# Performance work log

Hardware: AMD Instinct MI355X
Metric: run time of the kernel (lower is better)

Reference implementation:

```python
import jax, jax.numpy as jnp
import numpy as np
import math

HEADS = 16
D_MODEL = 1024
HEAD_DIM = D_MODEL // HEADS
B, S = 2, 2048


def setup_inputs() -> dict:
    key = jax.random.key(0)
    ks = jax.random.split(key, 12)
    sc = 1.0 / math.sqrt(D_MODEL)
    inp = {
        "query": jax.random.normal(ks[0], (B, S, D_MODEL), jnp.float32),
        "key_t": jax.random.normal(ks[1], (B, S, D_MODEL), jnp.float32),
        "value": jax.random.normal(ks[2], (B, S, D_MODEL), jnp.float32),
        "mask": jax.random.randint(ks[3], (B, 1, 1, S), 0, 2, jnp.int32),
        "Wq": jax.random.normal(ks[4], (D_MODEL, D_MODEL), jnp.float32) * sc,
        "bq": jnp.zeros((D_MODEL,), jnp.float32),
        "Wk": jax.random.normal(ks[5], (D_MODEL, D_MODEL), jnp.float32) * sc,
        "bk": jnp.zeros((D_MODEL,), jnp.float32),
        "Wv": jax.random.normal(ks[6], (D_MODEL, D_MODEL), jnp.float32) * sc,
        "bv": jnp.zeros((D_MODEL,), jnp.float32),
        "Wo": jax.random.normal(ks[7], (D_MODEL, D_MODEL), jnp.float32) * sc,
        "bo": jnp.zeros((D_MODEL,), jnp.float32),
    }
    return inp


def _split_heads(x):
    # [B, S, D] -> [B, H, S, Dh]
    b, s, _ = x.shape
    return x.reshape(b, s, HEADS, HEAD_DIM).transpose(0, 2, 1, 3)


def reference(query, key_t, value, mask, Wq, bq, Wk, bk, Wv, bv, Wo, bo):
    # Linear projections (torch Linear: x @ W.T + b)
    q = _split_heads(query @ Wq.T + bq)
    k = _split_heads(key_t @ Wk.T + bk)
    v = _split_heads(value @ Wv.T + bv)
    # Scaled dot-product attention; scale by sqrt(head_dim) = query.size(-1) after split
    scores = jnp.einsum("bhqd,bhkd->bhqk", q, k) / math.sqrt(HEAD_DIM)
    scores = jnp.where(mask == 0, jnp.float32(-1e9), scores)
    prob = jax.nn.softmax(scores, axis=-1)
    # dropout is identity at inference
    attn = jnp.einsum("bhqk,bhkd->bhqd", prob, v)
    # [B, H, S, Dh] -> [B, S, D]
    attn = attn.transpose(0, 2, 1, 3).reshape(query.shape[0], -1, D_MODEL)
    return attn @ Wo.T + bo
```

## Files before the change

### kernel.cpp

```cpp
#include <hip/hip_runtime.h>
#include <hip/hip_bf16.h>

typedef __bf16 bf16;
typedef __bf16 bf16x8 __attribute__((ext_vector_type(8)));
typedef __bf16 bf16x4 __attribute__((ext_vector_type(4)));
typedef float  f32x4  __attribute__((ext_vector_type(4)));
typedef float  f32x16 __attribute__((ext_vector_type(16)));

#define AS1 __attribute__((address_space(1)))
#define AS3 __attribute__((address_space(3)))

__device__ __forceinline__ void gload_lds16(const bf16* g, bf16* l) {
    __builtin_amdgcn_global_load_lds((const AS1 unsigned int*)g,
                                     (AS3 unsigned int*)l, 16, 0, 0);
}

__global__ __launch_bounds__(256) void cast8_k(
    const float* __restrict__ s0, const float* __restrict__ s1,
    const float* __restrict__ s2, const float* __restrict__ s3,
    const float* __restrict__ s4, const float* __restrict__ s5,
    const float* __restrict__ s6,
    bf16* __restrict__ d0, bf16* __restrict__ d1, bf16* __restrict__ d2,
    bf16* __restrict__ d3, bf16* __restrict__ d4, bf16* __restrict__ d5,
    bf16* __restrict__ d6,
    const int* __restrict__ m, float* __restrict__ mb,
    int n_big, int n_small) {
    int z = blockIdx.z;
    int i = (blockIdx.x * 256 + threadIdx.x) * 8;
    if (z == 7) {
        if (i >= 4096) return;
        int4 a = *(const int4*)(m + i);
        int4 b = *(const int4*)(m + i + 4);
        float4 o0, o1;
        o0.x = (a.x == 0) ? -1.442695e9f : -17.3123405f;
        o0.y = (a.y == 0) ? -1.442695e9f : -17.3123405f;
        o0.z = (a.z == 0) ? -1.442695e9f : -17.3123405f;
        o0.w = (a.w == 0) ? -1.442695e9f : -17.3123405f;
        o1.x = (b.x == 0) ? -1.442695e9f : -17.3123405f;
        o1.y = (b.y == 0) ? -1.442695e9f : -17.3123405f;
        o1.z = (b.z == 0) ? -1.442695e9f : -17.3123405f;
        o1.w = (b.w == 0) ? -1.442695e9f : -17.3123405f;
        *(float4*)(mb + i) = o0;
        *(float4*)(mb + i + 4) = o1;
        return;
    }
    const float* s = (z == 0) ? s0 : (z == 1) ? s1 : (z == 2) ? s2
                   : (z == 3) ? s3 : (z == 4) ? s4 : (z == 5) ? s5 : s6;
    bf16* d = (z == 0) ? d0 : (z == 1) ? d1 : (z == 2) ? d2
            : (z == 3) ? d3 : (z == 4) ? d4 : (z == 5) ? d5 : d6;
    int n = (z < 3) ? n_big : n_small;
    if (i >= n) return;
    float4 a = *(const float4*)(s + i);
    float4 b = *(const float4*)(s + i + 4);
    bf16x8 o;
    o[0] = (bf16)a.x; o[1] = (bf16)a.y; o[2] = (bf16)a.z; o[3] = (bf16)a.w;
    o[4] = (bf16)b.x; o[5] = (bf16)b.y; o[6] = (bf16)b.z; o[7] = (bf16)b.w;
    *(bf16x8*)(d + i) = o;
}

template <typename OUT_T, bool TRANS>
__device__ __forceinline__ void gemm32_core(
    bf16* Asm, bf16* Bsm,
    const bf16* __restrict__ A, const bf16* __restrict__ W,
    const float* __restrict__ bias, OUT_T* __restrict__ C,
    int m0, int n0, int N, int K) {
    const int lane = threadIdx.x & 63;
    const int w = threadIdx.x >> 6;
    const int l31 = lane & 31;
    const int h = lane >> 5;
    const int x7 = l31 & 7;
    const int srow = lane >> 3;
    const int scol = ((lane & 7) ^ srow) * 8;
    const int wm = (w & 1) * 64;
    const int wn = (w >> 1) * 64;

    f32x16 acc[2][2] = {};

    for (int k0 = 0; k0 < K; k0 += 64) {
#pragma unroll
        for (int c = 0; c < 4; ++c) {
            int r = w * 32 + c * 8;
            gload_lds16(A + (size_t)(m0 + r + srow) * K + k0 + scol, &Asm[r * 64]);
            gload_lds16(W + (size_t)(n0 + r + srow) * K + k0 + scol, &Bsm[r * 64]);
        }
        __syncthreads();
#pragma unroll
        for (int step = 0; step < 4; ++step) {
            bf16x8 af[2], bfv[2];
#pragma unroll
            for (int i = 0; i < 2; ++i)
                af[i] = *(const bf16x8*)&Asm[(wm + i * 32 + l31) * 64 +
                                             (((step * 2 + h) ^ x7) * 8)];
#pragma unroll
            for (int j = 0; j < 2; ++j)
                bfv[j] = *(const bf16x8*)&Bsm[(wn + j * 32 + l31) * 64 +
                                              (((step * 2 + h) ^ x7) * 8)];
#pragma unroll
            for (int i = 0; i < 2; ++i)
#pragma unroll
                for (int j = 0; j < 2; ++j)
                    acc[i][j] = TRANS
                        ? __builtin_amdgcn_mfma_f32_32x32x16_bf16(bfv[j], af[i],
                                                                  acc[i][j], 0, 0, 0)
                        : __builtin_amdgcn_mfma_f32_32x32x16_bf16(af[i], bfv[j],
                                                                  acc[i][j], 0, 0, 0);
        }
        __syncthreads();
    }
    if (!TRANS) {
#pragma unroll
        for (int i = 0; i < 2; ++i)
#pragma unroll
            for (int j = 0; j < 2; ++j) {
                int col = n0 + wn + j * 32 + l31;
                float bv = bias[col];
#pragma unroll
                for (int g = 0; g < 4; ++g)
#pragma unroll
                    for (int rr = 0; rr < 4; ++rr) {
                        int row = m0 + wm + i * 32 + rr + g * 8 + 4 * h;
                        C[(size_t)row * N + col] =
                            (OUT_T)(acc[i][j][g * 4 + rr] + bv);
                    }
            }
    } else {
#pragma unroll
        for (int i = 0; i < 2; ++i) {
            int s = m0 + wm + i * 32 + l31;
            int b = s >> 11;
            int sl = s & 2047;
            int sp = (sl & ~12) | ((sl & 4) << 1) | ((sl & 8) >> 1);
#pragma unroll
            for (int j = 0; j < 2; ++j)
#pragma unroll
                for (int g = 0; g < 4; ++g) {
                    float4 bv4 = *(const float4*)&bias[n0 + wn + j * 32 + g * 8 + 4 * h];
#pragma unroll
                    for (int rr = 0; rr < 4; ++rr) {
                        int n = n0 + wn + j * 32 + g * 8 + 4 * h + rr;
                        C[(size_t)(b * 1024 + n) * 2048 + sp] =
                            (OUT_T)(acc[i][j][g * 4 + rr] + (&bv4.x)[rr]);
                    }
                }
        }
    }
}

__global__ __launch_bounds__(256) void gemm_qkv(
    const bf16* __restrict__ qb, const bf16* __restrict__ kb, const bf16* __restrict__ vb,
    const bf16* __restrict__ Wq, const bf16* __restrict__ Wk, const bf16* __restrict__ Wv,
    const float* __restrict__ bq, const float* __restrict__ bk, const float* __restrict__ bv,
    bf16* __restrict__ Qp, bf16* __restrict__ Kp, bf16* __restrict__ VpT) {
    __shared__ bf16 Asm[128 * 64];
    __shared__ bf16 Bsm[128 * 64];
    const int id = blockIdx.x;
    const int g = id % 24;
    const int m0 = (id / 24) * 128;
    const int z = g >> 3;
    const int n0 = (g & 7) * 128;
    if (z == 2) {
        gemm32_core<bf16, true>(Asm, Bsm, vb, Wv, bv, VpT, m0, n0, 1024, 1024);
    } else {
        const bf16* A = (z == 0) ? qb : kb;
        const bf16* W = (z == 0) ? Wq : Wk;
        const float* bi = (z == 0) ? bq : bk;
        bf16* C = (z == 0) ? Qp : Kp;
        gemm32_core<bf16, false>(Asm, Bsm, A, W, bi, C, m0, n0, 1024, 1024);
    }
}

__global__ __launch_bounds__(256) void gemm_out_fused(
    const bf16* __restrict__ Op, const float* __restrict__ Lp,
    const bf16* __restrict__ W, const float* __restrict__ bias,
    float* __restrict__ C) {
    __shared__ bf16 Asm[64 * 64];
    __shared__ bf16 Bsm[128 * 64];
    const int id = blockIdx.x;
    const int m0 = (id & 63) * 64;
    const int n0 = (id >> 6) * 128;
    const int lane = threadIdx.x & 63;
    const int w = threadIdx.x >> 6;
    const int l31 = lane & 31;
    const int h = lane >> 5;
    const int x7 = l31 & 7;
    const int srow = lane >> 3;
    const int l7 = lane & 7;
    const int scol = (l7 ^ srow) * 8;
    const int wm = (w & 1) * 32;
    const int wn = (w >> 1) * 64;

    f32x16 acc[2] = {};

    for (int k0 = 0; k0 < 1024; k0 += 64) {
#pragma unroll
        for (int c = 0; c < 2; ++c) {
            int r = w * 16 + c * 8;
            int row = m0 + r + srow;
            int colb = k0 + scol;
            int b = row >> 11, q = row & 2047;
            int hh = colb >> 6, d = colb & 63;
            size_t l0i = (size_t)(b * 16 + hh) * 2048 + q;
            bf16x8 v0 = *(const bf16x8*)&Op[l0i * 64 + d];
            bf16x8 v1 = *(const bf16x8*)&Op[(l0i + 32 * 2048) * 64 + d];
            float inv = 1.0f / (Lp[l0i] + Lp[l0i + 32 * 2048]);
            bf16x8 o;
#pragma unroll
            for (int i = 0; i < 8; ++i)
                o[i] = (bf16)(((float)v0[i] + (float)v1[i]) * inv);
            *(bf16x8*)&Asm[(r + srow) * 64 + l7 * 8] = o;
        }
#pragma unroll
        for (int c = 0; c < 4; ++c) {
            int r = w * 32 + c * 8;
            gload_lds16(W + (size_t)(n0 + r + srow) * 1024 + k0 + scol, &Bsm[r * 64]);
        }
        __syncthreads();
#pragma unroll
        for (int step = 0; step < 4; ++step) {
            bf16x8 af = *(const bf16x8*)&Asm[(wm + l31) * 64 +
                                             (((step * 2 + h) ^ x7) * 8)];
            bf16x8 bfv[2];
#pragma unroll
            for (int j = 0; j < 2; ++j)
                bfv[j] = *(const bf16x8*)&Bsm[(wn + j * 32 + l31) * 64 +
                                              (((step * 2 + h) ^ x7) * 8)];
#pragma unroll
            for (int j = 0; j < 2; ++j)
                acc[j] = __builtin_amdgcn_mfma_f32_32x32x16_bf16(af, bfv[j],
                                                                 acc[j], 0, 0, 0);
        }
        __syncthreads();
    }
#pragma unroll
    for (int j = 0; j < 2; ++j) {
        int col = n0 + wn + j * 32 + l31;
        float bv = bias[col];
#pragma unroll
        for (int g = 0; g < 4; ++g)
#pragma unroll
            for (int rr = 0; rr < 4; ++rr) {
                int row = m0 + wm + rr + g * 8 + 4 * h;
                C[(size_t)row * 1024 + col] = acc[j][g * 4 + rr] + bv;
            }
    }
}

__global__ __launch_bounds__(256, 2) void attn_k(
    const bf16* __restrict__ Qp, const bf16* __restrict__ Kp,
    const bf16* __restrict__ VpT, const float* __restrict__ mb,
    bf16* __restrict__ Opart, float* __restrict__ Lpart) {
    __shared__ bf16 KV[2][2][64 * 64];
    const int g = blockIdx.x;
    const int qb = g >> 6;
    const int bh = (g & 63) >> 1;
    const int sp = g & 1;
    const int b = bh >> 4, hh = bh & 15;
    const int lane = threadIdx.x & 63, w = threadIdx.x >> 6;
    const int l31 = lane & 31, h = lane >> 5;
    const int x7 = l31 & 7;
    const int srow = lane >> 3, scol = ((lane & 7) ^ srow) * 8;
    const float SC = 0.125f * 1.44269504f;
    const int q0 = qb * 256;
    const int k0 = sp * 1024;

    const bf16* Kg = Kp + (size_t)(b * 2048) * 1024 + hh * 64;
    const bf16* Vg = VpT + (size_t)bh * 64 * 2048;
    const float* mbb = mb + b * 2048;

    auto stage = [&](int buf, int kt) {
#pragma unroll
        for (int c = 0; c < 2; ++c) {
            int r = w * 16 + c * 8;
            gload_lds16(Kg + (size_t)(kt + r + srow) * 1024 + scol,
                        &KV[buf][0][r * 64]);
            gload_lds16(Vg + (size_t)(r + srow) * 2048 + kt + scol,
                        &KV[buf][1][r * 64]);
        }
    };
    stage(0, k0);

    bf16x8 qf[2][4];
#pragma unroll
    for (int qg = 0; qg < 2; ++qg) {
        const bf16* Qbase =
            Qp + (size_t)(b * 2048 + q0 + w * 64 + qg * 32 + l31) * 1024 + hh * 64;
#pragma unroll
        for (int step = 0; step < 4; ++step)
            qf[qg][step] = *(const bf16x8*)(Qbase + step * 16 + h * 8);
    }

    f32x16 o[2][2] = {};
    float lsum[2] = {0.0f, 0.0f};

    for (int it = 0; it < 16; ++it) {
        __syncthreads();
        if (it < 15) stage((it + 1) & 1, k0 + (it + 1) * 64);
        const bf16* Ks = KV[it & 1][0];
        const bf16* Vs = KV[it & 1][1];
        const int kt = k0 + it * 64;

        bf16x8 pa[2][4];
#pragma unroll
        for (int kg = 0; kg < 2; ++kg) {
            f32x16 z0 = {}, z1 = {};
#pragma unroll
            for (int step = 0; step < 4; ++step) {
                bf16x8 kf = *(const bf16x8*)&Ks[(kg * 32 + l31) * 64 +
                                                (((step * 2 + h) ^ x7) * 8)];
                z0 = __builtin_amdgcn_mfma_f32_32x32x16_bf16(kf, qf[0][step], z0, 0, 0, 0);
                z1 = __builtin_amdgcn_mfma_f32_32x32x16_bf16(kf, qf[1][step], z1, 0, 0, 0);
            }
#pragma unroll
            for (int g = 0; g < 4; ++g) {
                float4 bia = *(const float4*)&mbb[kt + kg * 32 + g * 8 + 4 * h];
#pragma unroll
                for (int qg = 0; qg < 2; ++qg) {
                    const f32x16& z = qg ? z1 : z0;
                    float p0 = __builtin_amdgcn_exp2f(fmaf(z[g * 4 + 0], SC, bia.x));
                    float p1 = __builtin_amdgcn_exp2f(fmaf(z[g * 4 + 1], SC, bia.y));
                    float p2 = __builtin_amdgcn_exp2f(fmaf(z[g * 4 + 2], SC, bia.z));
                    float p3 = __builtin_amdgcn_exp2f(fmaf(z[g * 4 + 3], SC, bia.w));
                    lsum[qg] += (p0 + p1) + (p2 + p3);
                    bf16x8& pf = pa[qg][kg * 2 + (g >> 1)];
                    int jb = (g & 1) * 4;
                    pf[jb + 0] = (bf16)p0;
                    pf[jb + 1] = (bf16)p1;
                    pf[jb + 2] = (bf16)p2;
                    pf[jb + 3] = (bf16)p3;
                }
            }
        }
#pragma unroll
        for (int t = 0; t < 2; ++t)
#pragma unroll
            for (int kk = 0; kk < 4; ++kk) {
                bf16x8 vf = *(const bf16x8*)&Vs[(t * 32 + l31) * 64 +
                                                (((kk * 2 + h) ^ x7) * 8)];
                o[0][t] = __builtin_amdgcn_mfma_f32_32x32x16_bf16(pa[0][kk], vf, o[0][t], 0, 0, 0);
                o[1][t] = __builtin_amdgcn_mfma_f32_32x32x16_bf16(pa[1][kk], vf, o[1][t], 0, 0, 0);
            }
    }

    const size_t pbase = (size_t)(sp * 32 + bh) * 2048;
#pragma unroll
    for (int qg = 0; qg < 2; ++qg) {
        float ls = lsum[qg] + __shfl_xor(lsum[qg], 32, 64);
        if (h == 0)
            Lpart[pbase + q0 + w * 64 + qg * 32 + l31] = ls;
#pragma unroll
        for (int t = 0; t < 2; ++t)
#pragma unroll
            for (int g = 0; g < 4; ++g)
#pragma unroll
                for (int rr = 0; rr < 4; ++rr) {
                    int q = q0 + w * 64 + qg * 32 + rr + g * 8 + 4 * h;
                    Opart[(pbase + q) * 64 + t * 32 + l31] =
                        (bf16)o[qg][t][g * 4 + rr];
                }
    }
}

extern "C" void kernel_launch(void* const* d_in, const int* in_sizes, int n_in,
                              void* d_out, int out_size, void* d_ws, size_t ws_size,
                              hipStream_t stream) {
    const float* q   = (const float*)d_in[0];
    const float* kt  = (const float*)d_in[1];
    const float* v   = (const float*)d_in[2];
    const int* mask  = (const int*)d_in[3];
    const float* Wq  = (const float*)d_in[4];
    const float* bq  = (const float*)d_in[5];
    const float* Wk  = (const float*)d_in[6];
    const float* bk  = (const float*)d_in[7];
    const float* Wv  = (const float*)d_in[8];
    const float* bv  = (const float*)d_in[9];
    const float* Wo  = (const float*)d_in[10];
    const float* bo  = (const float*)d_in[11];
    float* out = (float*)d_out;

    char* ws = (char*)d_ws;
    const size_t SZ_IN = 4096ull * 1024 * 2;
    const size_t SZ_W  = 1024ull * 1024 * 2;
    bf16* qb  = (bf16*)(ws + 0 * SZ_IN);
    bf16* kb  = (bf16*)(ws + 1 * SZ_IN);
    bf16* vb  = (bf16*)(ws + 2 * SZ_IN);
    bf16* Wqb = (bf16*)(ws + 3 * SZ_IN);
    bf16* Wkb = (bf16*)(ws + 3 * SZ_IN + 1 * SZ_W);
    bf16* Wvb = (bf16*)(ws + 3 * SZ_IN + 2 * SZ_W);
    bf16* Wob = (bf16*)(ws + 3 * SZ_IN + 3 * SZ_W);
    bf16* Qp  = (bf16*)(ws + 3 * SZ_IN + 4 * SZ_W);
    bf16* Kp  = (bf16*)(ws + 4 * SZ_IN + 4 * SZ_W);
    bf16* VpT = (bf16*)(ws + 5 * SZ_IN + 4 * SZ_W);
    float* mb = (float*)(ws + 6 * SZ_IN + 4 * SZ_W);
    char*  p0 = ws + 6 * SZ_IN + 4 * SZ_W + (1 << 20);
    bf16* Opart = (bf16*)p0;
    float* Lpart = (float*)(p0 + 2ull * 32 * 2048 * 64 * 2);

    const int NIN = 4096 * 1024, NW = 1024 * 1024;
    cast8_k<<<dim3(NIN / 2048, 1, 8), 256, 0, stream>>>(
        q, kt, v, Wq, Wk, Wv, Wo, qb, kb, vb, Wqb, Wkb, Wvb, Wob,
        mask, mb, NIN, NW);

    gemm_qkv<<<dim3(768), 256, 0, stream>>>(qb, kb, vb, Wqb, Wkb, Wvb,
                                            bq, bk, bv, Qp, Kp, VpT);
    attn_k<<<dim3(512), 256, 0, stream>>>(Qp, Kp, VpT, mb, Opart, Lpart);
    gemm_out_fused<<<dim3(512), 256, 0, stream>>>(Opart, Lpart, Wob, bo, out);
}
```

Before: 226.6 us.

## Split attention keys four ways and flatten the cast launch grid

The attention kernel now splits the key range into four 512-key partitions instead of two, which doubles the grid to 1024 blocks and raises the launch bound to 4 blocks per CU for more occupancy. The output GEMM now sums four partial outputs and normalizers when it loads its A tile. The cast kernel moves from a 3D grid with idle blocks to a flat grid sized exactly to the work. The cost is twice the partial-output traffic and more reduction loads in the output GEMM, and the tighter launch bound may cause register spills.

```diff
diff --git a/kernel.cpp b/kernel.cpp
--- a/kernel.cpp
+++ b/kernel.cpp
@@ -15,7 +15,7 @@
                                      (AS3 unsigned int*)l, 16, 0, 0);
 }
 
-__global__ __launch_bounds__(256) void cast8_k(
+__global__ __launch_bounds__(256) void cast_flat_k(
     const float* __restrict__ s0, const float* __restrict__ s1,
     const float* __restrict__ s2, const float* __restrict__ s3,
     const float* __restrict__ s4, const float* __restrict__ s5,
@@ -23,12 +23,10 @@
     bf16* __restrict__ d0, bf16* __restrict__ d1, bf16* __restrict__ d2,
     bf16* __restrict__ d3, bf16* __restrict__ d4, bf16* __restrict__ d5,
     bf16* __restrict__ d6,
-    const int* __restrict__ m, float* __restrict__ mb,
-    int n_big, int n_small) {
-    int z = blockIdx.z;
-    int i = (blockIdx.x * 256 + threadIdx.x) * 8;
-    if (z == 7) {
-        if (i >= 4096) return;
+    const int* __restrict__ m, float* __restrict__ mb) {
+    int bx = blockIdx.x;
+    if (bx >= 8192) {
+        int i = (bx - 8192) * 2048 + threadIdx.x * 8;
         int4 a = *(const int4*)(m + i);
         int4 b = *(const int4*)(m + i + 4);
         float4 o0, o1;
@@ -44,12 +42,13 @@
         *(float4*)(mb + i + 4) = o1;
         return;
     }
+    int z, i;
+    if (bx < 6144) { z = bx >> 11; i = (bx & 2047) * 2048 + threadIdx.x * 8; }
+    else { int r = bx - 6144; z = 3 + (r >> 9); i = (r & 511) * 2048 + threadIdx.x * 8; }
     const float* s = (z == 0) ? s0 : (z == 1) ? s1 : (z == 2) ? s2
                    : (z == 3) ? s3 : (z == 4) ? s4 : (z == 5) ? s5 : s6;
     bf16* d = (z == 0) ? d0 : (z == 1) ? d1 : (z == 2) ? d2
             : (z == 3) ? d3 : (z == 4) ? d4 : (z == 5) ? d5 : d6;
-    int n = (z < 3) ? n_big : n_small;
-    if (i >= n) return;
     float4 a = *(const float4*)(s + i);
     float4 b = *(const float4*)(s + i + 4);
     bf16x8 o;
@@ -200,13 +199,20 @@
             int b = row >> 11, q = row & 2047;
             int hh = colb >> 6, d = colb & 63;
             size_t l0i = (size_t)(b * 16 + hh) * 2048 + q;
-            bf16x8 v0 = *(const bf16x8*)&Op[l0i * 64 + d];
-            bf16x8 v1 = *(const bf16x8*)&Op[(l0i + 32 * 2048) * 64 + d];
-            float inv = 1.0f / (Lp[l0i] + Lp[l0i + 32 * 2048]);
+            float a8[8] = {};
+            float l = 0.0f;
+#pragma unroll
+            for (int sp = 0; sp < 4; ++sp) {
+                size_t idx = l0i + (size_t)sp * 32 * 2048;
+                bf16x8 v = *(const bf16x8*)&Op[idx * 64 + d];
+                l += Lp[idx];
+#pragma unroll
+                for (int i = 0; i < 8; ++i) a8[i] += (float)v[i];
+            }
+            float inv = 1.0f / l;
             bf16x8 o;
 #pragma unroll
-            for (int i = 0; i < 8; ++i)
-                o[i] = (bf16)(((float)v0[i] + (float)v1[i]) * inv);
+            for (int i = 0; i < 8; ++i) o[i] = (bf16)(a8[i] * inv);
             *(bf16x8*)&Asm[(r + srow) * 64 + l7 * 8] = o;
         }
 #pragma unroll
@@ -245,15 +251,15 @@
     }
 }
 
-__global__ __launch_bounds__(256, 2) void attn_k(
+__global__ __launch_bounds__(256, 4) void attn_k(
     const bf16* __restrict__ Qp, const bf16* __restrict__ Kp,
     const bf16* __restrict__ VpT, const float* __restrict__ mb,
     bf16* __restrict__ Opart, float* __restrict__ Lpart) {
     __shared__ bf16 KV[2][2][64 * 64];
     const int g = blockIdx.x;
-    const int qb = g >> 6;
-    const int bh = (g & 63) >> 1;
-    const int sp = g & 1;
+    const int qb = g >> 7;
+    const int bh = (g & 127) >> 2;
+    const int sp = g & 3;
     const int b = bh >> 4, hh = bh & 15;
     const int lane = threadIdx.x & 63, w = threadIdx.x >> 6;
     const int l31 = lane & 31, h = lane >> 5;
@@ -261,7 +267,7 @@
     const int srow = lane >> 3, scol = ((lane & 7) ^ srow) * 8;
     const float SC = 0.125f * 1.44269504f;
     const int q0 = qb * 256;
-    const int k0 = sp * 1024;
+    const int k0 = sp * 512;
 
     const bf16* Kg = Kp + (size_t)(b * 2048) * 1024 + hh * 64;
     const bf16* Vg = VpT + (size_t)bh * 64 * 2048;
@@ -292,9 +298,9 @@
     f32x16 o[2][2] = {};
     float lsum[2] = {0.0f, 0.0f};
 
-    for (int it = 0; it < 16; ++it) {
+    for (int it = 0; it < 8; ++it) {
         __syncthreads();
-        if (it < 15) stage((it + 1) & 1, k0 + (it + 1) * 64);
+        if (it < 7) stage((it + 1) & 1, k0 + (it + 1) * 64);
         const bf16* Ks = KV[it & 1][0];
         const bf16* Vs = KV[it & 1][1];
         const int kt = k0 + it * 64;
@@ -393,15 +399,13 @@
     float* mb = (float*)(ws + 6 * SZ_IN + 4 * SZ_W);
     char*  p0 = ws + 6 * SZ_IN + 4 * SZ_W + (1 << 20);
     bf16* Opart = (bf16*)p0;
-    float* Lpart = (float*)(p0 + 2ull * 32 * 2048 * 64 * 2);
-
-    const int NIN = 4096 * 1024, NW = 1024 * 1024;
-    cast8_k<<<dim3(NIN / 2048, 1, 8), 256, 0, stream>>>(
-        q, kt, v, Wq, Wk, Wv, Wo, qb, kb, vb, Wqb, Wkb, Wvb, Wob,
-        mask, mb, NIN, NW);
+    float* Lpart = (float*)(p0 + 4ull * 32 * 2048 * 64 * 2);
+
+    cast_flat_k<<<dim3(8194), 256, 0, stream>>>(
+        q, kt, v, Wq, Wk, Wv, Wo, qb, kb, vb, Wqb, Wkb, Wvb, Wob, mask, mb);
 
     gemm_qkv<<<dim3(768), 256, 0, stream>>>(qb, kb, vb, Wqb, Wkb, Wvb,
                                             bq, bk, bv, Qp, Kp, VpT);
-    attn_k<<<dim3(512), 256, 0, stream>>>(Qp, Kp, VpT, mb, Opart, Lpart);
+    attn_k<<<dim3(1024), 256, 0, stream>>>(Qp, Kp, VpT, mb, Opart, Lpart);
     gemm_out_fused<<<dim3(512), 256, 0, stream>>>(Opart, Lpart, Wob, bo, out);
 }
```

Measured after the change: 416.2 us. +83.7%, slower.

## Fuse activation fp32->bf16 cast into QKV GEMM and halve attention query tile

Applied to the files above, without the earlier changes.

Removes the separate cast of the three large fp32 activation tensors to bf16; the QKV GEMM now loads fp32 rows, converts them in registers and writes them into swizzled LDS, so only weights and the mask are pre-cast. This avoids writing and re-reading about 24 MB of bf16 intermediates, but A-tile loads become synchronous register round trips instead of direct global-to-LDS loads, and each A tile is re-read in fp32 by every N-tile block. Separately, the attention kernel processes 32 query rows per wave instead of 64 and launches twice as many blocks, with the occupancy hint removed. That lowers register pressure and adds parallelism at the cost of loading the K/V tiles twice as often.

```diff
diff --git a/kernel.cpp b/kernel.cpp
--- a/kernel.cpp
+++ b/kernel.cpp
@@ -15,20 +15,15 @@
                                      (AS3 unsigned int*)l, 16, 0, 0);
 }
 
-__global__ __launch_bounds__(256) void cast8_k(
-    const float* __restrict__ s0, const float* __restrict__ s1,
-    const float* __restrict__ s2, const float* __restrict__ s3,
-    const float* __restrict__ s4, const float* __restrict__ s5,
-    const float* __restrict__ s6,
-    bf16* __restrict__ d0, bf16* __restrict__ d1, bf16* __restrict__ d2,
-    bf16* __restrict__ d3, bf16* __restrict__ d4, bf16* __restrict__ d5,
-    bf16* __restrict__ d6,
-    const int* __restrict__ m, float* __restrict__ mb,
-    int n_big, int n_small) {
-    int z = blockIdx.z;
-    int i = (blockIdx.x * 256 + threadIdx.x) * 8;
-    if (z == 7) {
-        if (i >= 4096) return;
+__global__ __launch_bounds__(256) void cast_w_k(
+    const float* __restrict__ s3, const float* __restrict__ s4,
+    const float* __restrict__ s5, const float* __restrict__ s6,
+    bf16* __restrict__ d3, bf16* __restrict__ d4,
+    bf16* __restrict__ d5, bf16* __restrict__ d6,
+    const int* __restrict__ m, float* __restrict__ mb) {
+    int bx = blockIdx.x;
+    if (bx >= 2048) {
+        int i = (bx - 2048) * 2048 + threadIdx.x * 8;
         int4 a = *(const int4*)(m + i);
         int4 b = *(const int4*)(m + i + 4);
         float4 o0, o1;
@@ -44,12 +39,10 @@
         *(float4*)(mb + i + 4) = o1;
         return;
     }
-    const float* s = (z == 0) ? s0 : (z == 1) ? s1 : (z == 2) ? s2
-                   : (z == 3) ? s3 : (z == 4) ? s4 : (z == 5) ? s5 : s6;
-    bf16* d = (z == 0) ? d0 : (z == 1) ? d1 : (z == 2) ? d2
-            : (z == 3) ? d3 : (z == 4) ? d4 : (z == 5) ? d5 : d6;
-    int n = (z < 3) ? n_big : n_small;
-    if (i >= n) return;
+    int z = bx >> 9;
+    int i = (bx & 511) * 2048 + threadIdx.x * 8;
+    const float* s = (z == 0) ? s3 : (z == 1) ? s4 : (z == 2) ? s5 : s6;
+    bf16* d = (z == 0) ? d3 : (z == 1) ? d4 : (z == 2) ? d5 : d6;
     float4 a = *(const float4*)(s + i);
     float4 b = *(const float4*)(s + i + 4);
     bf16x8 o;
@@ -61,7 +54,7 @@
 template <typename OUT_T, bool TRANS>
 __device__ __forceinline__ void gemm32_core(
     bf16* Asm, bf16* Bsm,
-    const bf16* __restrict__ A, const bf16* __restrict__ W,
+    const float* __restrict__ A, const bf16* __restrict__ W,
     const float* __restrict__ bias, OUT_T* __restrict__ C,
     int m0, int n0, int N, int K) {
     const int lane = threadIdx.x & 63;
@@ -73,14 +66,28 @@
     const int scol = ((lane & 7) ^ srow) * 8;
     const int wm = (w & 1) * 64;
     const int wn = (w >> 1) * 64;
+    const int arow = threadIdx.x >> 3;
+    const int achk = threadIdx.x & 7;
 
     f32x16 acc[2][2] = {};
 
     for (int k0 = 0; k0 < K; k0 += 64) {
+#pragma unroll
+        for (int ps = 0; ps < 4; ++ps) {
+            int rr = ps * 32 + arow;
+            const float* src = A + (size_t)(m0 + rr) * K + k0 + achk * 8;
+            float4 a0 = *(const float4*)src;
+            float4 a1 = *(const float4*)(src + 4);
+            bf16x8 ob;
+            ob[0] = (bf16)a0.x; ob[1] = (bf16)a0.y;
+            ob[2] = (bf16)a0.z; ob[3] = (bf16)a0.w;
+            ob[4] = (bf16)a1.x; ob[5] = (bf16)a1.y;
+            ob[6] = (bf16)a1.z; ob[7] = (bf16)a1.w;
+            *(bf16x8*)&Asm[rr * 64 + ((achk ^ (rr & 7)) * 8)] = ob;
+        }
 #pragma unroll
         for (int c = 0; c < 4; ++c) {
             int r = w * 32 + c * 8;
-            gload_lds16(A + (size_t)(m0 + r + srow) * K + k0 + scol, &Asm[r * 64]);
             gload_lds16(W + (size_t)(n0 + r + srow) * K + k0 + scol, &Bsm[r * 64]);
         }
         __syncthreads();
@@ -147,7 +154,8 @@
 }
 
 __global__ __launch_bounds__(256) void gemm_qkv(
-    const bf16* __restrict__ qb, const bf16* __restrict__ kb, const bf16* __restrict__ vb,
+    const float* __restrict__ qf32, const float* __restrict__ kf32,
+    const float* __restrict__ vf32,
     const bf16* __restrict__ Wq, const bf16* __restrict__ Wk, const bf16* __restrict__ Wv,
     const float* __restrict__ bq, const float* __restrict__ bk, const float* __restrict__ bv,
     bf16* __restrict__ Qp, bf16* __restrict__ Kp, bf16* __restrict__ VpT) {
@@ -159,9 +167,9 @@
     const int z = g >> 3;
     const int n0 = (g & 7) * 128;
     if (z == 2) {
-        gemm32_core<bf16, true>(Asm, Bsm, vb, Wv, bv, VpT, m0, n0, 1024, 1024);
+        gemm32_core<bf16, true>(Asm, Bsm, vf32, Wv, bv, VpT, m0, n0, 1024, 1024);
     } else {
-        const bf16* A = (z == 0) ? qb : kb;
+        const float* A = (z == 0) ? qf32 : kf32;
         const bf16* W = (z == 0) ? Wq : Wk;
         const float* bi = (z == 0) ? bq : bk;
         bf16* C = (z == 0) ? Qp : Kp;
@@ -245,7 +253,7 @@
     }
 }
 
-__global__ __launch_bounds__(256, 2) void attn_k(
+__global__ __launch_bounds__(256) void attn_k(
     const bf16* __restrict__ Qp, const bf16* __restrict__ Kp,
     const bf16* __restrict__ VpT, const float* __restrict__ mb,
     bf16* __restrict__ Opart, float* __restrict__ Lpart) {
@@ -260,7 +268,7 @@
     const int x7 = l31 & 7;
     const int srow = lane >> 3, scol = ((lane & 7) ^ srow) * 8;
     const float SC = 0.125f * 1.44269504f;
-    const int q0 = qb * 256;
+    const int q0 = qb * 128;
     const int k0 = sp * 1024;
 
     const bf16* Kg = Kp + (size_t)(b * 2048) * 1024 + hh * 64;
@@ -279,18 +287,17 @@
     };
     stage(0, k0);
 
-    bf16x8 qf[2][4];
-#pragma unroll
-    for (int qg = 0; qg < 2; ++qg) {
+    bf16x8 qf[4];
+    {
         const bf16* Qbase =
-            Qp + (size_t)(b * 2048 + q0 + w * 64 + qg * 32 + l31) * 1024 + hh * 64;
+            Qp + (size_t)(b * 2048 + q0 + w * 32 + l31) * 1024 + hh * 64;
 #pragma unroll
         for (int step = 0; step < 4; ++step)
-            qf[qg][step] = *(const bf16x8*)(Qbase + step * 16 + h * 8);
-    }
-
-    f32x16 o[2][2] = {};
-    float lsum[2] = {0.0f, 0.0f};
+            qf[step] = *(const bf16x8*)(Qbase + step * 16 + h * 8);
+    }
+
+    f32x16 o[2] = {};
+    float lsum = 0.0f;
 
     for (int it = 0; it < 16; ++it) {
         __syncthreads();
@@ -299,35 +306,30 @@
         const bf16* Vs = KV[it & 1][1];
         const int kt = k0 + it * 64;
 
-        bf16x8 pa[2][4];
+        bf16x8 pa[4];
 #pragma unroll
         for (int kg = 0; kg < 2; ++kg) {
-            f32x16 z0 = {}, z1 = {};
+            f32x16 z = {};
 #pragma unroll
             for (int step = 0; step < 4; ++step) {
                 bf16x8 kf = *(const bf16x8*)&Ks[(kg * 32 + l31) * 64 +
                                                 (((step * 2 + h) ^ x7) * 8)];
-                z0 = __builtin_amdgcn_mfma_f32_32x32x16_bf16(kf, qf[0][step], z0, 0, 0, 0);
-                z1 = __builtin_amdgcn_mfma_f32_32x32x16_bf16(kf, qf[1][step], z1, 0, 0, 0);
-            }
-#pragma unroll
-            for (int g = 0; g < 4; ++g) {
-                float4 bia = *(const float4*)&mbb[kt + kg * 32 + g * 8 + 4 * h];
-#pragma unroll
-                for (int qg = 0; qg < 2; ++qg) {
-                    const f32x16& z = qg ? z1 : z0;
-                    float p0 = __builtin_amdgcn_exp2f(fmaf(z[g * 4 + 0], SC, bia.x));
-                    float p1 = __builtin_amdgcn_exp2f(fmaf(z[g * 4 + 1], SC, bia.y));
-                    float p2 = __builtin_amdgcn_exp2f(fmaf(z[g * 4 + 2], SC, bia.z));
-                    float p3 = __builtin_amdgcn_exp2f(fmaf(z[g * 4 + 3], SC, bia.w));
-                    lsum[qg] += (p0 + p1) + (p2 + p3);
-                    bf16x8& pf = pa[qg][kg * 2 + (g >> 1)];
-                    int jb = (g & 1) * 4;
-                    pf[jb + 0] = (bf16)p0;
-                    pf[jb + 1] = (bf16)p1;
-                    pf[jb + 2] = (bf16)p2;
-                    pf[jb + 3] = (bf16)p3;
-                }
+                z = __builtin_amdgcn_mfma_f32_32x32x16_bf16(kf, qf[step], z, 0, 0, 0);
+            }
+#pragma unroll
+            for (int gg = 0; gg < 4; ++gg) {
+                float4 bia = *(const float4*)&mbb[kt + kg * 32 + gg * 8 + 4 * h];
+                float p0 = __builtin_amdgcn_exp2f(fmaf(z[gg * 4 + 0], SC, bia.x));
+                float p1 = __builtin_amdgcn_exp2f(fmaf(z[gg * 4 + 1], SC, bia.y));
+                float p2 = __builtin_amdgcn_exp2f(fmaf(z[gg * 4 + 2], SC, bia.z));
+                float p3 = __builtin_amdgcn_exp2f(fmaf(z[gg * 4 + 3], SC, bia.w));
+                lsum += (p0 + p1) + (p2 + p3);
+                bf16x8& pf = pa[kg * 2 + (gg >> 1)];
+                int jb = (gg & 1) * 4;
+                pf[jb + 0] = (bf16)p0;
+                pf[jb + 1] = (bf16)p1;
+                pf[jb + 2] = (bf16)p2;
+                pf[jb + 3] = (bf16)p3;
             }
         }
 #pragma unroll
@@ -336,28 +338,24 @@
             for (int kk = 0; kk < 4; ++kk) {
                 bf16x8 vf = *(const bf16x8*)&Vs[(t * 32 + l31) * 64 +
                                                 (((kk * 2 + h) ^ x7) * 8)];
-                o[0][t] = __builtin_amdgcn_mfma_f32_32x32x16_bf16(pa[0][kk], vf, o[0][t], 0, 0, 0);
-                o[1][t] = __builtin_amdgcn_mfma_f32_32x32x16_bf16(pa[1][kk], vf, o[1][t], 0, 0, 0);
+                o[t] = __builtin_amdgcn_mfma_f32_32x32x16_bf16(pa[kk], vf, o[t], 0, 0, 0);
             }
     }
 
     const size_t pbase = (size_t)(sp * 32 + bh) * 2048;
-#pragma unroll
-    for (int qg = 0; qg < 2; ++qg) {
-        float ls = lsum[qg] + __shfl_xor(lsum[qg], 32, 64);
-        if (h == 0)
-            Lpart[pbase + q0 + w * 64 + qg * 32 + l31] = ls;
-#pragma unroll
-        for (int t = 0; t < 2; ++t)
-#pragma unroll
-            for (int g = 0; g < 4; ++g)
-#pragma unroll
-                for (int rr = 0; rr < 4; ++rr) {
-                    int q = q0 + w * 64 + qg * 32 + rr + g * 8 + 4 * h;
-                    Opart[(pbase + q) * 64 + t * 32 + l31] =
-                        (bf16)o[qg][t][g * 4 + rr];
-                }
-    }
+    float ls = lsum + __shfl_xor(lsum, 32, 64);
+    if (h == 0)
+        Lpart[pbase + q0 + w * 32 + l31] = ls;
+#pragma unroll
+    for (int t = 0; t < 2; ++t)
+#pragma unroll
+        for (int gg = 0; gg < 4; ++gg)
+#pragma unroll
+            for (int rr = 0; rr < 4; ++rr) {
+                int q = q0 + w * 32 + rr + gg * 8 + 4 * h;
+                Opart[(pbase + q) * 64 + t * 32 + l31] =
+                    (bf16)o[t][gg * 4 + rr];
+            }
 }
 
 extern "C" void kernel_launch(void* const* d_in, const int* in_sizes, int n_in,
@@ -380,28 +378,23 @@
     char* ws = (char*)d_ws;
     const size_t SZ_IN = 4096ull * 1024 * 2;
     const size_t SZ_W  = 1024ull * 1024 * 2;
-    bf16* qb  = (bf16*)(ws + 0 * SZ_IN);
-    bf16* kb  = (bf16*)(ws + 1 * SZ_IN);
-    bf16* vb  = (bf16*)(ws + 2 * SZ_IN);
-    bf16* Wqb = (bf16*)(ws + 3 * SZ_IN);
-    bf16* Wkb = (bf16*)(ws + 3 * SZ_IN + 1 * SZ_W);
-    bf16* Wvb = (bf16*)(ws + 3 * SZ_IN + 2 * SZ_W);
-    bf16* Wob = (bf16*)(ws + 3 * SZ_IN + 3 * SZ_W);
-    bf16* Qp  = (bf16*)(ws + 3 * SZ_IN + 4 * SZ_W);
-    bf16* Kp  = (bf16*)(ws + 4 * SZ_IN + 4 * SZ_W);
-    bf16* VpT = (bf16*)(ws + 5 * SZ_IN + 4 * SZ_W);
-    float* mb = (float*)(ws + 6 * SZ_IN + 4 * SZ_W);
-    char*  p0 = ws + 6 * SZ_IN + 4 * SZ_W + (1 << 20);
+    bf16* Wqb = (bf16*)(ws + 0 * SZ_W);
+    bf16* Wkb = (bf16*)(ws + 1 * SZ_W);
+    bf16* Wvb = (bf16*)(ws + 2 * SZ_W);
+    bf16* Wob = (bf16*)(ws + 3 * SZ_W);
+    bf16* Qp  = (bf16*)(ws + 4 * SZ_W);
+    bf16* Kp  = (bf16*)(ws + 4 * SZ_W + 1 * SZ_IN);
+    bf16* VpT = (bf16*)(ws + 4 * SZ_W + 2 * SZ_IN);
+    float* mb = (float*)(ws + 4 * SZ_W + 3 * SZ_IN);
+    char*  p0 = ws + 4 * SZ_W + 3 * SZ_IN + (1 << 20);
     bf16* Opart = (bf16*)p0;
     float* Lpart = (float*)(p0 + 2ull * 32 * 2048 * 64 * 2);
 
-    const int NIN = 4096 * 1024, NW = 1024 * 1024;
-    cast8_k<<<dim3(NIN / 2048, 1, 8), 256, 0, stream>>>(
-        q, kt, v, Wq, Wk, Wv, Wo, qb, kb, vb, Wqb, Wkb, Wvb, Wob,
-        mask, mb, NIN, NW);
-
-    gemm_qkv<<<dim3(768), 256, 0, stream>>>(qb, kb, vb, Wqb, Wkb, Wvb,
+    cast_w_k<<<dim3(2050), 256, 0, stream>>>(
+        Wq, Wk, Wv, Wo, Wqb, Wkb, Wvb, Wob, mask, mb);
+
+    gemm_qkv<<<dim3(768), 256, 0, stream>>>(q, kt, v, Wqb, Wkb, Wvb,
                                             bq, bk, bv, Qp, Kp, VpT);
-    attn_k<<<dim3(512), 256, 0, stream>>>(Qp, Kp, VpT, mb, Opart, Lpart);
+    attn_k<<<dim3(1024), 256, 0, stream>>>(Qp, Kp, VpT, mb, Opart, Lpart);
     gemm_out_fused<<<dim3(512), 256, 0, stream>>>(Opart, Lpart, Wob, bo, out);
 }
```

Result: slower. 268.1 us (+18.3%).
